# Performance work log

Measured on AMD Instinct MI355X. Metric: run time of the kernel, lower is better.

## Reference

```python
import jax, jax.numpy as jnp
import numpy as np
import math

B_, L_, D_, N_ = 8, 2048, 1024, 64


def _ln(x, g, b):
    m = jnp.mean(x, axis=-1, keepdims=True)
    v = jnp.mean((x - m) ** 2, axis=-1, keepdims=True)
    return (x - m) / jnp.sqrt(v + 1e-5) * g + b


def _ssm_kernel(A, Bp, Cp, Dp, L):
    # diagonal SSM: lambda = exp(diag(A)); k[l] = C diag(lambda)^l B + D  -> shape (L,)
    a = jnp.diagonal(A)                                   # (N,)
    powers = jnp.exp(jnp.arange(L)[:, None] * a[None, :])  # (L, N) = lambda^l
    return powers @ (Bp[:, 0] * Cp[0]) + Dp[0]             # (L,)


def _causal_conv(h, k):
    # y[:, t, :] = sum_{j<=t} k[j] * h[:, t-j, :]  via zero-padded FFT (same math, O(L log L))
    L = h.shape[1]
    n = 2 * L
    Hf = jnp.fft.rfft(h, n=n, axis=1)
    Kf = jnp.fft.rfft(k, n=n)
    return jnp.fft.irfft(Hf * Kf[None, :, None], n=n, axis=1)[:, :L]


def _timestep_embedding(t, dim):
    half = dim // 2
    freqs = jnp.exp(jnp.arange(half) * (-math.log(10000.0) / (half - 1)))
    ang = t[:, None] * freqs[None, :]
    return jnp.concatenate([jnp.sin(ang), jnp.cos(ang)], axis=1)  # (B, dim)


def _conv1d(x, w, b):
    # x: (B, C, L), w: (O, I, 3) torch layout, padding=1
    y = jax.lax.conv_general_dilated(x, w, (1,), [(1, 1)],
                                     dimension_numbers=('NCH', 'OIH', 'NCH'))
    return y + b[None, :, None]


def setup_inputs():
    key = jax.random.key(0)
    ks = jax.random.split(key, 26)
    d = {}
    d['x'] = jax.random.normal(ks[0], (B_, L_, D_), jnp.float32)
    d['t'] = jax.random.uniform(ks[1], (B_,), jnp.float32) * 1000.0
    d['beta1'] = jax.random.uniform(ks[2], (1,), jnp.float32)
    d['beta2'] = jax.random.uniform(ks[3], (1,), jnp.float32)
    sc = 1.0 / math.sqrt(D_)
    d['Wi'] = jax.random.normal(ks[4], (D_, D_), jnp.float32) * sc
    d['bi'] = jnp.zeros((D_,), jnp.float32)
    d['Wo'] = jax.random.normal(ks[5], (D_, D_), jnp.float32) * sc
    d['bo'] = jnp.zeros((D_,), jnp.float32)
    d['w1'] = jax.random.normal(ks[6], (D_, D_, 3), jnp.float32) * 0.02
    d['bc1'] = jnp.zeros((D_,), jnp.float32)
    d['w2'] = jax.random.normal(ks[7], (D_, D_, 3), jnp.float32) * 0.02
    d['bc2'] = jnp.zeros((D_,), jnp.float32)
    d['g1'] = jnp.ones((D_,), jnp.float32)
    d['b1'] = jnp.zeros((D_,), jnp.float32)
    d['g2'] = jnp.ones((D_,), jnp.float32)
    d['b2'] = jnp.zeros((D_,), jnp.float32)
    # SSM params (std 0.001 on A keeps exp(l*a) bounded for l up to L)
    d['Af'] = jax.random.normal(ks[8], (N_, N_), jnp.float32) * 0.001
    d['Bf'] = jax.random.normal(ks[9], (N_, 1), jnp.float32) * 0.01
    d['Cf'] = jax.random.normal(ks[10], (1, N_), jnp.float32) * 0.01
    d['Df'] = jax.random.normal(ks[11], (1,), jnp.float32) * 0.01
    d['Ab'] = jax.random.normal(ks[12], (N_, N_), jnp.float32) * 0.001
    d['Bb'] = jax.random.normal(ks[13], (N_, 1), jnp.float32) * 0.01
    d['Cb'] = jax.random.normal(ks[14], (1, N_), jnp.float32) * 0.01
    d['Db'] = jax.random.normal(ks[15], (1,), jnp.float32) * 0.01
    return d


def reference(x, t, beta1, beta2, Wi, bi, Wo, bo, w1, bc1, w2, bc2,
              g1, b1, g2, b2, Af, Bf, Cf, Df, Ab, Bb, Cb, Db):
    Bsz, L, D = x.shape
    h = x @ Wi + bi
    h = _ln(h, g1, b1)
    # local conv branch
    hT = jnp.transpose(h, (0, 2, 1))                 # (B, D, L)
    co = jax.nn.silu(_conv1d(hT, w1, bc1))
    co = _conv1d(co, w2, bc2)
    conv_out = jnp.transpose(co, (0, 2, 1))          # (B, L, D)
    # bidirectional SSM global convolutions
    kf = _ssm_kernel(Af, Bf, Cf, Df, L)
    h_fwd = _causal_conv(h, kf)
    kb = _ssm_kernel(Ab, Bb, Cb, Db, L)
    h_bwd = jnp.flip(_causal_conv(jnp.flip(h, axis=1), kb), axis=1)
    # timestep-conditioned mixing
    noise_scale = jax.nn.sigmoid(_timestep_embedding(t, D))[:, None, :]  # (B,1,D)
    h = h_fwd * (beta1[0] * noise_scale) + h_bwd * (beta2[0] * noise_scale) + conv_out
    h = h @ Wo + bo
    h = _ln(h, g2, b2)
    return x + h
```

## Files before the change

### kernel.cpp

```cpp
#include <hip/hip_runtime.h>

#define Bq 8
#define Lq 2048
#define Dq 1024
#define LPq 2050

typedef unsigned short u16;
typedef __attribute__((ext_vector_type(8))) short bf16x8;
typedef __attribute__((ext_vector_type(4))) float f32x4;

__device__ __forceinline__ u16 f2bf(float f) {
  unsigned u = __float_as_uint(f);
  u += 0x7FFFu + ((u >> 16) & 1u);
  return (u16)(u >> 16);
}
__device__ __forceinline__ float bf2f(u16 s) {
  return __uint_as_float(((unsigned)s) << 16);
}
__device__ __forceinline__ void gld16(const u16* g, u16* l) {
  __builtin_amdgcn_global_load_lds((const __attribute__((address_space(1))) void*)g,
                                   (__attribute__((address_space(3))) void*)l, 16, 0, 0);
}


__global__ __launch_bounds__(256) void prep_small(
    const float* __restrict__ t, const float* __restrict__ beta1, const float* __restrict__ beta2,
    const float* __restrict__ Af, const float* __restrict__ Bf, const float* __restrict__ Cf, const float* __restrict__ Df,
    const float* __restrict__ Ab, const float* __restrict__ Bb, const float* __restrict__ Cb, const float* __restrict__ Db,
    float* __restrict__ kf, float* __restrict__ kb,
    float* __restrict__ c1, float* __restrict__ c2,
    u16* __restrict__ hpad, u16* __restrict__ copad) {
  int tid = blockIdx.x * 256 + threadIdx.x;
  if (blockIdx.x < 8) {
    int l = tid;
    float sf = Df[0], sb = Db[0];
    for (int n = 0; n < 64; n++) {
      sf += __expf((float)l * Af[n * 64 + n]) * (Bf[n] * Cf[n]);
      sb += __expf((float)l * Ab[n * 64 + n]) * (Bb[n] * Cb[n]);
    }
    kf[l] = sf; kb[l] = sb;
  } else if (blockIdx.x < 40) {
    int i = tid - 2048;
    int b = i >> 10, d = i & 1023;
    float tb = t[b];
    float e;
    if (d < 512) {
      float f = __expf((float)d * (-logf(10000.f) / 511.f));
      e = sinf(tb * f);
    } else {
      float f = __expf((float)(d - 512) * (-logf(10000.f) / 511.f));
      e = cosf(tb * f);
    }
    float ns = 1.f / (1.f + __expf(-e));
    c1[i] = beta1[0] * ns;
    c2[i] = beta2[0] * ns;
  } else {
    int i = tid - 10240;
    if (i < 32768) {
      int d = i & 1023;
      int j = i >> 10;
      int arr = j & 1, r = (j >> 1) & 1, b = j >> 2;
      size_t off = (size_t)b * LPq * Dq + (r ? (size_t)(LPq - 1) * Dq : 0) + d;
      if (arr == 0) hpad[off] = 0;
      else          copad[off] = 0;
    }
  }
}

__global__ __launch_bounds__(256) void mega_prep(
    const float* __restrict__ x, u16* __restrict__ xb,
    const float* __restrict__ Wi, u16* __restrict__ wit,
    const float* __restrict__ Wo, u16* __restrict__ wot,
    const float* __restrict__ w1, u16* __restrict__ w1t,
    const float* __restrict__ w2, u16* __restrict__ w2t,
    const float* __restrict__ kf, const float* __restrict__ kb,
    u16* __restrict__ Tf, u16* __restrict__ Tb) {
  int bid = blockIdx.x, tid = threadIdx.x;
  if (bid < 8192) {
    size_t i = ((size_t)bid * 256 + tid) * 8;
    float4 a = *(const float4*)(x + i);
    float4 b = *(const float4*)(x + i + 4);
    u16 o[8] = {f2bf(a.x), f2bf(a.y), f2bf(a.z), f2bf(a.w),
                f2bf(b.x), f2bf(b.y), f2bf(b.z), f2bf(b.w)};
    *(bf16x8*)(xb + i) = *(const bf16x8*)o;
  } else if (bid < 8704) {
    __shared__ float tile[64][65];
    const float* W = (bid < 8448) ? Wi : Wo;
    u16* Wt = (bid < 8448) ? wit : wot;
    int b2 = (bid < 8448) ? bid - 8192 : bid - 8448;
    int bx = b2 & 15, by = b2 >> 4;
    int tx = tid & 63, tw = tid >> 6;
    for (int r = tw; r < 64; r += 4)
      tile[r][tx] = W[(size_t)(by * 64 + r) * 1024 + bx * 64 + tx];
    __syncthreads();
    for (int r = tw; r < 64; r += 4)
      Wt[(size_t)(bx * 64 + r) * 1024 + by * 64 + tx] = f2bf(tile[tx][r]);
  } else if (bid < 14848) {
    const float* w = (bid < 11776) ? w1 : w2;
    u16* Wt = (bid < 11776) ? w1t : w2t;
    int vb = (bid < 11776) ? bid - 8704 : bid - 11776;
    int base = (vb * 256 + tid) * 4;
    int o = base / 3072, rem = base % 3072;
    int dt = rem >> 10, i0 = rem & 1023;
    const float* src = w + (size_t)o * 3072 + dt;
    ushort4 v;
    v.x = f2bf(src[(i0 + 0) * 3]);
    v.y = f2bf(src[(i0 + 1) * 3]);
    v.z = f2bf(src[(i0 + 2) * 3]);
    v.w = f2bf(src[(i0 + 3) * 3]);
    *(ushort4*)(Wt + base) = v;
  } else {
    int idx = (bid - 14848) * 256 + tid;
    int tr = idx >> 9, j0 = (idx & 511) * 4;
    ushort4 vf, vb4;
    int j;
    j = j0 + 0; vf.x = (tr >= j) ? f2bf(kf[tr - j]) : (u16)0; vb4.x = (j >= tr) ? f2bf(kb[j - tr]) : (u16)0;
    j = j0 + 1; vf.y = (tr >= j) ? f2bf(kf[tr - j]) : (u16)0; vb4.y = (j >= tr) ? f2bf(kb[j - tr]) : (u16)0;
    j = j0 + 2; vf.z = (tr >= j) ? f2bf(kf[tr - j]) : (u16)0; vb4.z = (j >= tr) ? f2bf(kb[j - tr]) : (u16)0;
    j = j0 + 3; vf.w = (tr >= j) ? f2bf(kf[tr - j]) : (u16)0; vb4.w = (j >= tr) ? f2bf(kb[j - tr]) : (u16)0;
    *(ushort4*)(Tf + (size_t)tr * 2048 + j0) = vf;
    *(ushort4*)(Tb + (size_t)tr * 2048 + j0) = vb4;
  }
}

__global__ __launch_bounds__(256) void trans_h(const u16* __restrict__ hpad, u16* __restrict__ ht) {
  __shared__ u16 tile[64][66];
  int b = blockIdx.z;
  int lt = blockIdx.x * 64, dt = blockIdx.y * 64;
  int tx = threadIdx.x & 15, ty = threadIdx.x >> 4;
  const u16* src = hpad + (size_t)b * LPq * Dq + (size_t)(lt + 1 + ty) * Dq + dt + tx * 4;
#pragma unroll
  for (int i = 0; i < 4; i++) {
    int r = ty + i * 16;
    ushort4 v = *(const ushort4*)(src + (size_t)i * 16 * Dq);
    tile[tx * 4 + 0][r] = v.x;
    tile[tx * 4 + 1][r] = v.y;
    tile[tx * 4 + 2][r] = v.z;
    tile[tx * 4 + 3][r] = v.w;
  }
  __syncthreads();
#pragma unroll
  for (int i = 0; i < 4; i++) {
    int d = ty + i * 16;
    ushort4 v;
    v.x = tile[d][tx * 4 + 0];
    v.y = tile[d][tx * 4 + 1];
    v.z = tile[d][tx * 4 + 2];
    v.w = tile[d][tx * 4 + 3];
    *(ushort4*)(ht + ((size_t)b * Dq + dt + d) * Lq + lt + tx * 4) = v;
  }
}


__global__ __launch_bounds__(256) void ln1_k(const u16* __restrict__ h0, u16* __restrict__ hpad,
                                             const float* __restrict__ g, const float* __restrict__ be) {
  int w = threadIdx.x >> 6, lane = threadIdx.x & 63;
  int r = blockIdx.x * 4 + w;
  int d0 = lane * 16;
  const u16* hp = h0 + (size_t)r * 1024 + d0;
  bf16x8 va = *(const bf16x8*)hp;
  bf16x8 vb = *(const bf16x8*)(hp + 8);
  float v[16];
#pragma unroll
  for (int i = 0; i < 8; i++) { v[i] = bf2f((u16)va[i]); v[8 + i] = bf2f((u16)vb[i]); }
  float s = 0.f, q = 0.f;
#pragma unroll
  for (int i = 0; i < 16; i++) { s += v[i]; q += v[i] * v[i]; }
#pragma unroll
  for (int o = 32; o > 0; o >>= 1) { s += __shfl_xor(s, o); q += __shfl_xor(q, o); }
  float mean = s * (1.f / 1024.f);
  float rstd = rsqrtf(q * (1.f / 1024.f) - mean * mean + 1e-5f);
  const float4* g4 = (const float4*)(g + d0);
  const float4* b4 = (const float4*)(be + d0);
  u16 o16[16];
#pragma unroll
  for (int i = 0; i < 4; i++) {
    float4 gv = g4[i], bv = b4[i];
    o16[i * 4 + 0] = f2bf((v[i * 4 + 0] - mean) * rstd * gv.x + bv.x);
    o16[i * 4 + 1] = f2bf((v[i * 4 + 1] - mean) * rstd * gv.y + bv.y);
    o16[i * 4 + 2] = f2bf((v[i * 4 + 2] - mean) * rstd * gv.z + bv.z);
    o16[i * 4 + 3] = f2bf((v[i * 4 + 3] - mean) * rstd * gv.w + bv.w);
  }
  int b_ = r >> 11, l = r & 2047;
  u16* dst = hpad + ((size_t)b_ * LPq + l + 1) * Dq + d0;
  *(bf16x8*)dst = *(const bf16x8*)o16;
  *(bf16x8*)(dst + 8) = *(const bf16x8*)(o16 + 8);
}

__global__ __launch_bounds__(256) void ln2_k(const u16* __restrict__ hp, const float* __restrict__ x,
                                             const float* __restrict__ g, const float* __restrict__ be,
                                             float* __restrict__ out) {
  int w = threadIdx.x >> 6, lane = threadIdx.x & 63;
  size_t r = (size_t)blockIdx.x * 4 + w;
  int d0 = lane * 16;
  size_t base = r * 1024 + d0;
  const u16* h = hp + base;
  bf16x8 va = *(const bf16x8*)h;
  bf16x8 vb = *(const bf16x8*)(h + 8);
  float v[16];
#pragma unroll
  for (int i = 0; i < 8; i++) { v[i] = bf2f((u16)va[i]); v[8 + i] = bf2f((u16)vb[i]); }
  float s = 0.f, q = 0.f;
#pragma unroll
  for (int i = 0; i < 16; i++) { s += v[i]; q += v[i] * v[i]; }
#pragma unroll
  for (int o = 32; o > 0; o >>= 1) { s += __shfl_xor(s, o); q += __shfl_xor(q, o); }
  float mean = s * (1.f / 1024.f);
  float rstd = rsqrtf(q * (1.f / 1024.f) - mean * mean + 1e-5f);
  const float4* g4 = (const float4*)(g + d0);
  const float4* b4 = (const float4*)(be + d0);
  const float4* x4 = (const float4*)(x + base);
  float4* o4 = (float4*)(out + base);
#pragma unroll
  for (int i = 0; i < 4; i++) {
    float4 gv = g4[i], bv = b4[i], xv = x4[i];
    float4 o;
    o.x = xv.x + (v[i * 4 + 0] - mean) * rstd * gv.x + bv.x;
    o.y = xv.y + (v[i * 4 + 1] - mean) * rstd * gv.y + bv.y;
    o.z = xv.z + (v[i * 4 + 2] - mean) * rstd * gv.z + bv.z;
    o.w = xv.w + (v[i * 4 + 3] - mean) * rstd * gv.w + bv.w;
    o4[i] = o;
  }
}

__device__ __forceinline__ void gemm_core(const u16* __restrict__ Ab, int lda,
                                          const u16* __restrict__ Bb, int ldb,
                                          int ks, int NS, u16* lds,
                                          f32x4 (&acc)[8][4]) {
  const int t = threadIdx.x;
  const int lane = t & 63, w = t >> 6;
  const int g = w >> 2, j = w & 3;
  const int p1 = t >> 3;
  const int c1 = (t & 7) ^ (p1 & 7);
  const int row1 = (p1 << 1) | (c1 >> 2), f1 = c1 & 3;
  const int q2 = t + 512;
  const int p2 = q2 >> 3;
  const int c2 = (q2 & 7) ^ (p2 & 7);
  const int row2 = (p2 << 1) | (c2 >> 2), f2 = c2 & 3;
  const int aoff1 = row1 * lda + f1 * 8;
  const int aoff2 = row2 * lda + f2 * 8;
  const int boff1 = row1 * ldb + f1 * 8;
  const int boff2 = row2 * ldb + f2 * 8;
  u16* wA1 = lds + t * 8;
  u16* wA2 = lds + 4096 + t * 8;
  u16* wB1 = lds + 8192 + t * 8;
  u16* wB2 = lds + 12288 + t * 8;
  const int frow = lane & 15, fkc = lane >> 4;
  const int arow = g * 128 + frow;
  const int pa = arow >> 1, ca = ((arow & 1) << 2) | fkc;
  const int abase = pa * 64 + ((ca ^ (pa & 7)) << 3);
  const int brow = j * 64 + frow;
  const int pb = brow >> 1, cb = ((brow & 1) << 2) | fkc;
  const int bbase = 8192 + pb * 64 + ((cb ^ (pb & 7)) << 3);

#define STAGE_A(s_) { int sl_ = ((s_) & 3) * 16384; const u16* g_ = Ab + ks + (s_) * 32; \
    gld16(g_ + aoff1, wA1 + sl_); gld16(g_ + aoff2, wA2 + sl_); }
#define STAGE_B(s_) { int sl_ = ((s_) & 3) * 16384; const u16* g_ = Bb + ks + (s_) * 32; \
    gld16(g_ + boff1, wB1 + sl_); gld16(g_ + boff2, wB2 + sl_); }

  STAGE_A(0); STAGE_B(0);
  STAGE_A(1); STAGE_B(1);
  STAGE_A(2); STAGE_B(2);

  for (int s = 0; s < NS; s++) {
    const u16* sl = lds + (s & 3) * 16384;
    if (s <= NS - 3)      { asm volatile("s_waitcnt vmcnt(8)" ::: "memory"); }
    else if (s == NS - 2) { asm volatile("s_waitcnt vmcnt(4)" ::: "memory"); }
    else                  { asm volatile("s_waitcnt vmcnt(0)" ::: "memory"); }
    asm volatile("s_barrier" ::: "memory");
    if (s + 3 < NS) STAGE_A(s + 3);
    bf16x8 bq[4], af[4];
#pragma unroll
    for (int nf = 0; nf < 4; nf++) bq[nf] = *(const bf16x8*)(sl + bbase + nf * 512);
#pragma unroll
    for (int mf = 0; mf < 4; mf++) af[mf] = *(const bf16x8*)(sl + abase + mf * 512);
    __builtin_amdgcn_s_setprio(1);
#pragma unroll
    for (int mf = 0; mf < 4; mf++)
#pragma unroll
      for (int nf = 0; nf < 4; nf++)
        acc[mf][nf] = __builtin_amdgcn_mfma_f32_16x16x32_bf16(af[mf], bq[nf], acc[mf][nf], 0, 0, 0);
    __builtin_amdgcn_s_setprio(0);
    if (s + 3 < NS) STAGE_B(s + 3);
#pragma unroll
    for (int mf = 0; mf < 4; mf++) af[mf] = *(const bf16x8*)(sl + abase + 2048 + mf * 512);
    __builtin_amdgcn_s_setprio(1);
#pragma unroll
    for (int mf = 0; mf < 4; mf++)
#pragma unroll
      for (int nf = 0; nf < 4; nf++)
        acc[4 + mf][nf] = __builtin_amdgcn_mfma_f32_16x16x32_bf16(af[mf], bq[nf], acc[4 + mf][nf], 0, 0, 0);
    __builtin_amdgcn_s_setprio(0);
  }
#undef STAGE_A
#undef STAGE_B
}

template <int MODE>
__global__ __launch_bounds__(512, 2) void gemm8(
    const u16* __restrict__ A, int lda, long abstr,
    const u16* __restrict__ Bw, int ldb,
    u16* __restrict__ Out, long obstr,
    const u16* __restrict__ aux,
    const float* __restrict__ bias, int K, int nbm) {
  __shared__ __align__(16) u16 lds[65536];
  int mb = blockIdx.x % nbm, nb = blockIdx.x / nbm;
  int m0 = mb * 256, n0 = nb * 256;
  int batch = m0 >> 11, r0 = m0 & 2047;
  const u16* Ab = A + (size_t)batch * abstr + (size_t)r0 * lda;
  const u16* Bb = Bw + (size_t)n0 * ldb;
  f32x4 acc[8][4] = {};
  gemm_core(Ab, lda, Bb, ldb, 0, K >> 5, lds, acc);
  int lane = threadIdx.x & 63, w = threadIdx.x >> 6;
  int g = w >> 2, j = w & 3;
  int frow = lane & 15;
  u16* ob = Out + (size_t)batch * obstr;
  const u16* ab2 = (MODE == 3) ? aux + (size_t)batch * obstr : nullptr;
#pragma unroll
  for (int mf = 0; mf < 8; mf++) {
    int row = r0 + g * 128 + mf * 16 + ((lane >> 4) << 2);
#pragma unroll
    for (int nf = 0; nf < 4; nf++) {
      int col = n0 + j * 64 + nf * 16 + frow;
      float bv = bias[col];
      size_t base = (size_t)row * 1024 + col;
      f32x4 a = acc[mf][nf];
#pragma unroll
      for (int i = 0; i < 4; i++) {
        float v = a[i] + bv;
        if (MODE == 1) v = v / (1.f + __expf(-v));
        if (MODE == 3) v += bf2f(ob[base + (size_t)i * 1024]) + bf2f(ab2[base + (size_t)i * 1024]);
        ob[base + (size_t)i * 1024] = f2bf(v);
      }
    }
  }
}

__global__ __launch_bounds__(512, 2) void mix8(
    const u16* __restrict__ hpad, const u16* __restrict__ w1t,
    u16* __restrict__ co, const float* __restrict__ bc1,
    const u16* __restrict__ Tf, const u16* __restrict__ Tb,
    const u16* __restrict__ Ht,
    const float* __restrict__ c1, const float* __restrict__ c2,
    u16* __restrict__ outF, u16* __restrict__ outB) {
  __shared__ __align__(16) u16 lds[65536];
  const long PSTR = (long)LPq * 1024;
  int id = blockIdx.x;
  int lane = threadIdx.x & 63, w = threadIdx.x >> 6;
  int g = w >> 2, j = w & 3;
  int frow = lane & 15;
  if (id < 256) {
    int mb = id & 63, nb = id >> 6;
    int m0 = mb * 256, n0 = nb * 256;
    int batch = m0 >> 11, r0 = m0 & 2047;
    const u16* Ab = hpad + (size_t)batch * PSTR + (size_t)r0 * 1024;
    const u16* Bb = w1t + (size_t)n0 * 3072;
    f32x4 acc[8][4] = {};
    gemm_core(Ab, 1024, Bb, 3072, 0, 96, lds, acc);
    u16* ob = co + (size_t)batch * PSTR;
#pragma unroll
    for (int mf = 0; mf < 8; mf++) {
      int row = r0 + g * 128 + mf * 16 + ((lane >> 4) << 2);
#pragma unroll
      for (int nf = 0; nf < 4; nf++) {
        int col = n0 + j * 64 + nf * 16 + frow;
        float bv = bc1[col];
        size_t base = (size_t)row * 1024 + col;
        f32x4 a = acc[mf][nf];
#pragma unroll
        for (int i = 0; i < 4; i++) {
          float v = a[i] + bv;
          v = v / (1.f + __expf(-v));
          ob[base + (size_t)i * 1024] = f2bf(v);
        }
      }
    }
  } else {
    int rr = id - 256;
    int dir = rr >> 8, r = rr & 255;
    int mb = dir ? (r & 7) : (7 - (r & 7));
    int nb = r >> 3;
    int m0 = mb * 256, n0 = nb * 256;
    int ks = dir ? m0 : 0;
    int ke = dir ? 2048 : m0 + 256;
    const u16* Tm = dir ? Tb : Tf;
    const u16* Ab = Tm + (size_t)m0 * 2048;
    const u16* Bb = Ht + (size_t)n0 * 2048;
    f32x4 acc[8][4] = {};
    gemm_core(Ab, 2048, Bb, 2048, ks, (ke - ks) >> 5, lds, acc);
    const float* cs = dir ? c2 : c1;
    u16* out = dir ? outB : outF;
#pragma unroll
    for (int mf = 0; mf < 8; mf++) {
      int row = m0 + g * 128 + mf * 16 + ((lane >> 4) << 2);
#pragma unroll
      for (int nf = 0; nf < 4; nf++) {
        int col = n0 + j * 64 + nf * 16 + frow;
        int b = col >> 10, d = col & 1023;
        float cv = cs[col];
        u16* op = out + ((size_t)b * Lq + row) * 1024 + d;
        f32x4 a = acc[mf][nf];
#pragma unroll
        for (int i = 0; i < 4; i++)
          op[(size_t)i * 1024] = f2bf(a[i] * cv);
      }
    }
  }
}


extern "C" void kernel_launch(void* const* d_in, const int* in_sizes, int n_in,
                              void* d_out, int out_size, void* d_ws, size_t ws_size,
                              hipStream_t stream) {
  const float* x   = (const float*)d_in[0];
  const float* tt  = (const float*)d_in[1];
  const float* be1 = (const float*)d_in[2];
  const float* be2 = (const float*)d_in[3];
  const float* Wi  = (const float*)d_in[4];
  const float* bi  = (const float*)d_in[5];
  const float* Wo  = (const float*)d_in[6];
  const float* bo  = (const float*)d_in[7];
  const float* w1  = (const float*)d_in[8];
  const float* bc1 = (const float*)d_in[9];
  const float* w2  = (const float*)d_in[10];
  const float* bc2 = (const float*)d_in[11];
  const float* g1  = (const float*)d_in[12];
  const float* b1  = (const float*)d_in[13];
  const float* g2  = (const float*)d_in[14];
  const float* b2  = (const float*)d_in[15];
  const float* Af  = (const float*)d_in[16];
  const float* Bf  = (const float*)d_in[17];
  const float* Cf  = (const float*)d_in[18];
  const float* Df  = (const float*)d_in[19];
  const float* Ab  = (const float*)d_in[20];
  const float* Bb  = (const float*)d_in[21];
  const float* Cb  = (const float*)d_in[22];
  const float* Db  = (const float*)d_in[23];

  char* p = (char*)d_ws;
  constexpr size_t SZ_h0   = (size_t)16384 * 1024 * 2;
  constexpr size_t SZ_hpad = (size_t)Bq * LPq * Dq * 2;
  constexpr size_t SZ_ht   = (size_t)Bq * Dq * Lq * 2;
  constexpr size_t SZ_hmix = (size_t)16384 * 1024 * 2;
  constexpr size_t SZ_T    = (size_t)2048 * 2048 * 2;
  constexpr size_t SZ_wt   = (size_t)1024 * 1024 * 2;
  constexpr size_t SZ_w3t  = (size_t)1024 * 3072 * 2;

  size_t off = 0;
  u16* h0    = (u16*)(p + off); off += SZ_h0;
  u16* hpad  = (u16*)(p + off); off += SZ_hpad;
  u16* ht    = (u16*)(p + off); off += SZ_ht;
  u16* copad = (u16*)(p + off); off += SZ_hpad;
  u16* hmixF = (u16*)(p + off); off += SZ_hmix;
  u16* Tf    = (u16*)(p + off); off += SZ_T;
  u16* Tb    = (u16*)(p + off); off += SZ_T;
  u16* wit   = (u16*)(p + off); off += SZ_wt;
  u16* wot   = (u16*)(p + off); off += SZ_wt;
  u16* w1t   = (u16*)(p + off); off += SZ_w3t;
  u16* w2t   = (u16*)(p + off); off += SZ_w3t;
  float* kf  = (float*)(p + off); off += 8192;
  float* kb  = (float*)(p + off); off += 8192;
  float* c1  = (float*)(p + off); off += 32768;
  float* c2  = (float*)(p + off); off += 32768;
  u16* xb    = hmixF;
  u16* hmixB = h0;

  const long BSTR = (long)2048 * 1024;
  const long PSTR = (long)LPq * 1024;

  prep_small<<<dim3(168), dim3(256), 0, stream>>>(tt, be1, be2, Af, Bf, Cf, Df,
                                                  Ab, Bb, Cb, Db, kf, kb, c1, c2, hpad, copad);
  mega_prep<<<dim3(18944), dim3(256), 0, stream>>>(x, xb, Wi, wit, Wo, wot,
                                                   w1, w1t, w2, w2t, kf, kb, Tf, Tb);

  gemm8<0><<<dim3(256), dim3(512), 0, stream>>>(xb, 1024, BSTR, wit, 1024, h0, BSTR, nullptr, bi, 1024, 64);
  ln1_k<<<dim3(4096), dim3(256), 0, stream>>>(h0, hpad, g1, b1);
  trans_h<<<dim3(32, 16, 8), dim3(256), 0, stream>>>(hpad, ht);
  mix8<<<dim3(768), dim3(512), 0, stream>>>(hpad, w1t, copad + 1024, bc1,
                                            Tf, Tb, ht, c1, c2, hmixF, hmixB);
  gemm8<3><<<dim3(256), dim3(512), 0, stream>>>(copad, 1024, PSTR, w2t, 3072, hmixF, BSTR, hmixB, bc2, 3072, 64);
  gemm8<0><<<dim3(256), dim3(512), 0, stream>>>(hmixF, 1024, BSTR, wot, 1024, h0, BSTR, nullptr, bo, 1024, 64);
  ln2_k<<<dim3(4096), dim3(256), 0, stream>>>(h0, x, g2, b2, (float*)d_out);
}
```

Before: 496.9 us.

## Merge forward and backward SSM Toeplitz matrices into one beta-weighted matrix

The two triangular Toeplitz matrices are folded into one dense matrix, with beta1 and beta2 applied to the kernels inside it. The bidirectional SSM then becomes a single full-K GEMM scaled by the noise factor, writing one output buffer. This removes one 32MB intermediate write and its later read in the conv2 epilogue, and cuts total K-work slightly compared with the two triangular passes. In exchange, the merged mix8 launch is split into separate conv1 and SSM GEMM launches, which loses the combined scheduling of the 768-block grid.

After: 446.6 us. 1.11x faster.

```diff
diff --git a/kernel.cpp b/kernel.cpp
--- a/kernel.cpp
+++ b/kernel.cpp
@@ -24,11 +24,11 @@
 
 
 __global__ __launch_bounds__(256) void prep_small(
-    const float* __restrict__ t, const float* __restrict__ beta1, const float* __restrict__ beta2,
+    const float* __restrict__ t,
     const float* __restrict__ Af, const float* __restrict__ Bf, const float* __restrict__ Cf, const float* __restrict__ Df,
     const float* __restrict__ Ab, const float* __restrict__ Bb, const float* __restrict__ Cb, const float* __restrict__ Db,
     float* __restrict__ kf, float* __restrict__ kb,
-    float* __restrict__ c1, float* __restrict__ c2,
+    float* __restrict__ ns,
     u16* __restrict__ hpad, u16* __restrict__ copad) {
   int tid = blockIdx.x * 256 + threadIdx.x;
   if (blockIdx.x < 8) {
@@ -51,9 +51,7 @@
       float f = __expf((float)(d - 512) * (-logf(10000.f) / 511.f));
       e = cosf(tb * f);
     }
-    float ns = 1.f / (1.f + __expf(-e));
-    c1[i] = beta1[0] * ns;
-    c2[i] = beta2[0] * ns;
+    ns[i] = 1.f / (1.f + __expf(-e));
   } else {
     int i = tid - 10240;
     if (i < 32768) {
@@ -74,7 +72,8 @@
     const float* __restrict__ w1, u16* __restrict__ w1t,
     const float* __restrict__ w2, u16* __restrict__ w2t,
     const float* __restrict__ kf, const float* __restrict__ kb,
-    u16* __restrict__ Tf, u16* __restrict__ Tb) {
+    const float* __restrict__ be1, const float* __restrict__ be2,
+    u16* __restrict__ Tm) {
   int bid = blockIdx.x, tid = threadIdx.x;
   if (bid < 8192) {
     size_t i = ((size_t)bid * 256 + tid) * 8;
@@ -112,14 +111,17 @@
   } else {
     int idx = (bid - 14848) * 256 + tid;
     int tr = idx >> 9, j0 = (idx & 511) * 4;
-    ushort4 vf, vb4;
-    int j;
-    j = j0 + 0; vf.x = (tr >= j) ? f2bf(kf[tr - j]) : (u16)0; vb4.x = (j >= tr) ? f2bf(kb[j - tr]) : (u16)0;
-    j = j0 + 1; vf.y = (tr >= j) ? f2bf(kf[tr - j]) : (u16)0; vb4.y = (j >= tr) ? f2bf(kb[j - tr]) : (u16)0;
-    j = j0 + 2; vf.z = (tr >= j) ? f2bf(kf[tr - j]) : (u16)0; vb4.z = (j >= tr) ? f2bf(kb[j - tr]) : (u16)0;
-    j = j0 + 3; vf.w = (tr >= j) ? f2bf(kf[tr - j]) : (u16)0; vb4.w = (j >= tr) ? f2bf(kb[j - tr]) : (u16)0;
-    *(ushort4*)(Tf + (size_t)tr * 2048 + j0) = vf;
-    *(ushort4*)(Tb + (size_t)tr * 2048 + j0) = vb4;
+    float b1v = be1[0], b2v = be2[0];
+    ushort4 v;
+#pragma unroll
+    for (int q = 0; q < 4; q++) {
+      int j = j0 + q;
+      float vv = 0.f;
+      if (tr >= j) vv += b1v * kf[tr - j];
+      if (j >= tr) vv += b2v * kb[j - tr];
+      ((u16*)&v)[q] = f2bf(vv);
+    }
+    *(ushort4*)(Tm + (size_t)tr * 2048 + j0) = v;
   }
 }
 
@@ -301,7 +303,6 @@
     const u16* __restrict__ A, int lda, long abstr,
     const u16* __restrict__ Bw, int ldb,
     u16* __restrict__ Out, long obstr,
-    const u16* __restrict__ aux,
     const float* __restrict__ bias, int K, int nbm) {
   __shared__ __align__(16) u16 lds[65536];
   int mb = blockIdx.x % nbm, nb = blockIdx.x / nbm;
@@ -315,7 +316,6 @@
   int g = w >> 2, j = w & 3;
   int frow = lane & 15;
   u16* ob = Out + (size_t)batch * obstr;
-  const u16* ab2 = (MODE == 3) ? aux + (size_t)batch * obstr : nullptr;
 #pragma unroll
   for (int mf = 0; mf < 8; mf++) {
     int row = r0 + g * 128 + mf * 16 + ((lane >> 4) << 2);
@@ -329,81 +329,39 @@
       for (int i = 0; i < 4; i++) {
         float v = a[i] + bv;
         if (MODE == 1) v = v / (1.f + __expf(-v));
-        if (MODE == 3) v += bf2f(ob[base + (size_t)i * 1024]) + bf2f(ab2[base + (size_t)i * 1024]);
+        if (MODE == 2) v += bf2f(ob[base + (size_t)i * 1024]);
         ob[base + (size_t)i * 1024] = f2bf(v);
       }
     }
   }
 }
 
-__global__ __launch_bounds__(512, 2) void mix8(
-    const u16* __restrict__ hpad, const u16* __restrict__ w1t,
-    u16* __restrict__ co, const float* __restrict__ bc1,
-    const u16* __restrict__ Tf, const u16* __restrict__ Tb,
-    const u16* __restrict__ Ht,
-    const float* __restrict__ c1, const float* __restrict__ c2,
-    u16* __restrict__ outF, u16* __restrict__ outB) {
+__global__ __launch_bounds__(512, 2) void ssm8(
+    const u16* __restrict__ Tm, const u16* __restrict__ Ht,
+    const float* __restrict__ ns, u16* __restrict__ out) {
   __shared__ __align__(16) u16 lds[65536];
-  const long PSTR = (long)LPq * 1024;
-  int id = blockIdx.x;
+  int mb = blockIdx.x & 7, nb = blockIdx.x >> 3;
+  int m0 = mb * 256, n0 = nb * 256;
+  const u16* Ab = Tm + (size_t)m0 * 2048;
+  const u16* Bb = Ht + (size_t)n0 * 2048;
+  f32x4 acc[8][4] = {};
+  gemm_core(Ab, 2048, Bb, 2048, 0, 64, lds, acc);
   int lane = threadIdx.x & 63, w = threadIdx.x >> 6;
   int g = w >> 2, j = w & 3;
   int frow = lane & 15;
-  if (id < 256) {
-    int mb = id & 63, nb = id >> 6;
-    int m0 = mb * 256, n0 = nb * 256;
-    int batch = m0 >> 11, r0 = m0 & 2047;
-    const u16* Ab = hpad + (size_t)batch * PSTR + (size_t)r0 * 1024;
-    const u16* Bb = w1t + (size_t)n0 * 3072;
-    f32x4 acc[8][4] = {};
-    gemm_core(Ab, 1024, Bb, 3072, 0, 96, lds, acc);
-    u16* ob = co + (size_t)batch * PSTR;
-#pragma unroll
-    for (int mf = 0; mf < 8; mf++) {
-      int row = r0 + g * 128 + mf * 16 + ((lane >> 4) << 2);
-#pragma unroll
-      for (int nf = 0; nf < 4; nf++) {
-        int col = n0 + j * 64 + nf * 16 + frow;
-        float bv = bc1[col];
-        size_t base = (size_t)row * 1024 + col;
-        f32x4 a = acc[mf][nf];
-#pragma unroll
-        for (int i = 0; i < 4; i++) {
-          float v = a[i] + bv;
-          v = v / (1.f + __expf(-v));
-          ob[base + (size_t)i * 1024] = f2bf(v);
-        }
-      }
-    }
-  } else {
-    int rr = id - 256;
-    int dir = rr >> 8, r = rr & 255;
-    int mb = dir ? (r & 7) : (7 - (r & 7));
-    int nb = r >> 3;
-    int m0 = mb * 256, n0 = nb * 256;
-    int ks = dir ? m0 : 0;
-    int ke = dir ? 2048 : m0 + 256;
-    const u16* Tm = dir ? Tb : Tf;
-    const u16* Ab = Tm + (size_t)m0 * 2048;
-    const u16* Bb = Ht + (size_t)n0 * 2048;
-    f32x4 acc[8][4] = {};
-    gemm_core(Ab, 2048, Bb, 2048, ks, (ke - ks) >> 5, lds, acc);
-    const float* cs = dir ? c2 : c1;
-    u16* out = dir ? outB : outF;
-#pragma unroll
-    for (int mf = 0; mf < 8; mf++) {
-      int row = m0 + g * 128 + mf * 16 + ((lane >> 4) << 2);
-#pragma unroll
-      for (int nf = 0; nf < 4; nf++) {
-        int col = n0 + j * 64 + nf * 16 + frow;
-        int b = col >> 10, d = col & 1023;
-        float cv = cs[col];
-        u16* op = out + ((size_t)b * Lq + row) * 1024 + d;
-        f32x4 a = acc[mf][nf];
-#pragma unroll
-        for (int i = 0; i < 4; i++)
-          op[(size_t)i * 1024] = f2bf(a[i] * cv);
-      }
+#pragma unroll
+  for (int mf = 0; mf < 8; mf++) {
+    int row = m0 + g * 128 + mf * 16 + ((lane >> 4) << 2);
+#pragma unroll
+    for (int nf = 0; nf < 4; nf++) {
+      int col = n0 + j * 64 + nf * 16 + frow;
+      int b = col >> 10, d = col & 1023;
+      float cv = ns[col];
+      u16* op = out + ((size_t)b * Lq + row) * 1024 + d;
+      f32x4 a = acc[mf][nf];
+#pragma unroll
+      for (int i = 0; i < 4; i++)
+        op[(size_t)i * 1024] = f2bf(a[i] * cv);
     }
   }
 }
@@ -452,33 +410,30 @@
   u16* ht    = (u16*)(p + off); off += SZ_ht;
   u16* copad = (u16*)(p + off); off += SZ_hpad;
   u16* hmixF = (u16*)(p + off); off += SZ_hmix;
-  u16* Tf    = (u16*)(p + off); off += SZ_T;
-  u16* Tb    = (u16*)(p + off); off += SZ_T;
+  u16* Tmat  = (u16*)(p + off); off += SZ_T;
   u16* wit   = (u16*)(p + off); off += SZ_wt;
   u16* wot   = (u16*)(p + off); off += SZ_wt;
   u16* w1t   = (u16*)(p + off); off += SZ_w3t;
   u16* w2t   = (u16*)(p + off); off += SZ_w3t;
   float* kf  = (float*)(p + off); off += 8192;
   float* kb  = (float*)(p + off); off += 8192;
-  float* c1  = (float*)(p + off); off += 32768;
-  float* c2  = (float*)(p + off); off += 32768;
+  float* nsb = (float*)(p + off); off += 32768;
   u16* xb    = hmixF;
-  u16* hmixB = h0;
 
   const long BSTR = (long)2048 * 1024;
   const long PSTR = (long)LPq * 1024;
 
-  prep_small<<<dim3(168), dim3(256), 0, stream>>>(tt, be1, be2, Af, Bf, Cf, Df,
-                                                  Ab, Bb, Cb, Db, kf, kb, c1, c2, hpad, copad);
+  prep_small<<<dim3(168), dim3(256), 0, stream>>>(tt, Af, Bf, Cf, Df,
+                                                  Ab, Bb, Cb, Db, kf, kb, nsb, hpad, copad);
   mega_prep<<<dim3(18944), dim3(256), 0, stream>>>(x, xb, Wi, wit, Wo, wot,
-                                                   w1, w1t, w2, w2t, kf, kb, Tf, Tb);
-
-  gemm8<0><<<dim3(256), dim3(512), 0, stream>>>(xb, 1024, BSTR, wit, 1024, h0, BSTR, nullptr, bi, 1024, 64);
+                                                   w1, w1t, w2, w2t, kf, kb, be1, be2, Tmat);
+
+  gemm8<0><<<dim3(256), dim3(512), 0, stream>>>(xb, 1024, BSTR, wit, 1024, h0, BSTR, bi, 1024, 64);
   ln1_k<<<dim3(4096), dim3(256), 0, stream>>>(h0, hpad, g1, b1);
   trans_h<<<dim3(32, 16, 8), dim3(256), 0, stream>>>(hpad, ht);
-  mix8<<<dim3(768), dim3(512), 0, stream>>>(hpad, w1t, copad + 1024, bc1,
-                                            Tf, Tb, ht, c1, c2, hmixF, hmixB);
-  gemm8<3><<<dim3(256), dim3(512), 0, stream>>>(copad, 1024, PSTR, w2t, 3072, hmixF, BSTR, hmixB, bc2, 3072, 64);
-  gemm8<0><<<dim3(256), dim3(512), 0, stream>>>(hmixF, 1024, BSTR, wot, 1024, h0, BSTR, nullptr, bo, 1024, 64);
+  gemm8<1><<<dim3(256), dim3(512), 0, stream>>>(hpad, 1024, PSTR, w1t, 3072, copad + 1024, PSTR, bc1, 3072, 64);
+  ssm8<<<dim3(256), dim3(512), 0, stream>>>(Tmat, ht, nsb, hmixF);
+  gemm8<2><<<dim3(256), dim3(512), 0, stream>>>(copad, 1024, PSTR, w2t, 3072, hmixF, BSTR, bc2, 3072, 64);
+  gemm8<0><<<dim3(256), dim3(512), 0, stream>>>(hmixF, 1024, BSTR, wot, 1024, h0, BSTR, bo, 1024, 64);
   ln2_k<<<dim3(4096), dim3(256), 0, stream>>>(h0, x, g2, b2, (float*)d_out);
 }
```
